# Optimization experiments

Hardware: AMD Instinct MI355X
Metric: run time of the kernel (lower is better)

The kernel has to match this reference:

```python
import jax, jax.numpy as jnp
import numpy as np

B, NV, NL, D, H = 32, 512, 256, 1024, 4096


def _ffn(x, w1, b1, w2, b2):
    # torch FFN: linear2(relu(linear1(x))); weights stored as [in, out]
    return jnp.maximum(x @ w1 + b1, 0.0) @ w2 + b2


def setup_inputs() -> dict:
    key = jax.random.key(0)
    ks = jax.random.split(key, 12)
    s_in = 1.0 / np.sqrt(D)
    s_h = 1.0 / np.sqrt(H)
    return {
        "V": jax.random.normal(ks[0], (B, NV, D), jnp.float32),
        "L": jax.random.normal(ks[1], (B, NL, D), jnp.float32),
        "v_mask": jnp.ones((B, NV), jnp.float32),
        "l_mask": jnp.ones((B, NL), jnp.float32),
        "w1_V": jax.random.normal(ks[2], (D, H), jnp.float32) * s_in,
        "b1_V": jnp.zeros((H,), jnp.float32),
        "w2_V": jax.random.normal(ks[3], (H, D), jnp.float32) * s_h,
        "b2_V": jnp.zeros((D,), jnp.float32),
        "w1_L": jax.random.normal(ks[4], (D, H), jnp.float32) * s_in,
        "b1_L": jnp.zeros((H,), jnp.float32),
        "w2_L": jax.random.normal(ks[5], (H, D), jnp.float32) * s_h,
        "b2_L": jnp.zeros((D,), jnp.float32),
    }


def reference(V, L, v_mask, l_mask, w1_V, b1_V, w2_V, b2_V, w1_L, b1_L, w2_L, b2_L):
    # masks are unused in the original forward
    fV_V = _ffn(V, w1_V, b1_V, w2_V, b2_V)  # [B, NV, D] = ffn_V(V)
    fL_L = _ffn(L, w1_L, b1_L, w2_L, b2_L)  # [B, NL, D] = ffn_L(L)
    fL_V = _ffn(V, w1_L, b1_L, w2_L, b2_L)  # [B, NV, D] = ffn_L(V) (as in source)
    scale = 1.0 / jnp.sqrt(jnp.asarray(V.shape[-1], V.dtype))
    A_LV = jnp.einsum('bnd,bmd->bnm', fV_V, fL_L) * scale  # [B, NV, NL]
    A_VV = jnp.einsum('bnd,bmd->bnm', fV_V, fL_V) * scale  # [B, NV, NV]
    A = jnp.concatenate([A_LV, A_VV], axis=-1)             # [B, NV, NL+NV]
    # softmax over dim=1 (rows), as in the source
    attn = jax.nn.softmax(A, axis=1)
    KV = jnp.concatenate([fL_L, fV_V], axis=1)              # [B, NL+NV, D]
    V_next = jnp.einsum('bnk,bkd->bnd', attn, KV)           # [B, NV, D]
    return (A, V_next)
```

## Files before the change

kernel.cpp:

```cpp
#include <hip/hip_runtime.h>
#include <stdint.h>

#define B_   32
#define NV_  512
#define NL_  256
#define D_   1024
#define H_   4096
#define KTOT 768
#define SCALE_ 0.03125f

typedef __attribute__((ext_vector_type(8))) __bf16 bf8_t;
typedef __attribute__((ext_vector_type(4))) float f32x4;

__device__ __forceinline__ unsigned short f2bf(float f) {
    unsigned u = __float_as_uint(f);
    u += 0x7FFFu + ((u >> 16) & 1u);
    return (unsigned short)(u >> 16);
}
__device__ __forceinline__ unsigned pk2(float lo, float hi) {
    return (unsigned)f2bf(lo) | ((unsigned)f2bf(hi) << 16);
}

__device__ __forceinline__ void gl_lds16(const void* g, const void* lds) {
    __builtin_amdgcn_global_load_lds(
        (const __attribute__((address_space(1))) unsigned int*)(uintptr_t)g,
        (__attribute__((address_space(3))) unsigned int*)(unsigned)(uintptr_t)lds,
        16, 0, 0);
}

#define SBAR() asm volatile("s_barrier" ::: "memory")
#define VMC4() asm volatile("s_waitcnt vmcnt(4)" ::: "memory")
#define VMC0() asm volatile("s_waitcnt vmcnt(0)" ::: "memory")

template<int EPI>
__global__ __launch_bounds__(512, 1)
void gemm256(const unsigned short* __restrict__ Ab, long sAz, int lda,
             const unsigned short* __restrict__ Bb, long sBz, int ldb,
             const float* __restrict__ bias,
             unsigned short* __restrict__ Cp, long sCz, int ldc, int K,
             int nx, int ntile, int tpc)
{
    extern __shared__ unsigned char lds[];
    unsigned char* const ldsA = lds;
    unsigned char* const ldsB = lds + 65536;

    const int tid = threadIdx.x;
    const int w = tid >> 6, l = tid & 63;
    const int wr = w >> 2, wc = w & 3;
    const int lrow = l & 15;
    const int kg = l >> 4;

    int t_, z;
    {
        const int bid = blockIdx.x;
        if (tpc > 0) { const int r = bid >> 3, c = bid & 7; z = r / tpc; t_ = c * tpc + r % tpc; }
        else         { z = bid / ntile; t_ = bid - z * ntile; }
    }
    const int n0 = (t_ % nx) * 256, m0 = (t_ / nx) * 256;

    const unsigned short* A  = Ab + (long)z * sAz;
    const unsigned short* Bg = Bb + (long)z * sBz;

    const int srow = tid >> 3;
    const int scol = ((tid & 7) * 8) ^ ((srow & 7) << 3);
    const int ntk = K >> 6;

    const int cs0 = (((l >> 4) * 16)) ^ ((l & 7) << 4);
    const int cs1 = (64 + ((l >> 4) * 16)) ^ ((l & 7) << 4);

    const unsigned short* const sp0 = Bg + (long)(n0 +   0 + srow) * ldb + scol;
    const unsigned short* const sp1 = Bg + (long)(n0 + 128 + srow) * ldb + scol;
    const unsigned short* const sp2 = A  + (long)(m0 +   0 + srow) * lda + scol;
    const unsigned short* const sp3 = A  + (long)(m0 + 128 + srow) * lda + scol;
    const long stB = (long)64 * ldb, stA = (long)64 * lda;

    f32x4 acc[8][4];
#pragma unroll
    for (int i = 0; i < 8; ++i)
#pragma unroll
        for (int j = 0; j < 4; ++j) acc[i][j] = (f32x4){0.f, 0.f, 0.f, 0.f};

#define STG(tau, part) do {                                                   \
        const int buf_ = (tau) & 1;                                           \
        const int kt_ = ((tau) < ntk ? (tau) : ntk - 1);                      \
        if ((part) < 2) {                                                     \
            const unsigned short* s_ = ((part) == 0 ? sp0 : sp1) + (long)kt_ * 64; \
            unsigned char* d_ = ldsB + (buf_ * 2 + (part)) * 16384 + w * 1024;\
            gl_lds16(s_, d_); gl_lds16(s_ + stB, d_ + 8192);                  \
        } else {                                                              \
            const unsigned short* s_ = ((part) == 2 ? sp2 : sp3) + (long)kt_ * 64; \
            unsigned char* d_ = ldsA + (buf_ * 2 + (part) - 2) * 16384 + w * 1024; \
            gl_lds16(s_, d_); gl_lds16(s_ + stA, d_ + 8192);                  \
        } } while (0)

    auto rdA = [&](int buf, int mf, int cs) -> bf8_t {
        return *(const bf8_t*)(ldsA + (buf * 2 + wr) * 16384 + (mf * 16 + lrow) * 128 + cs);
    };
    auto rdB = [&](int buf, int nf, int cs) -> bf8_t {
        return *(const bf8_t*)(ldsB + (buf * 2 + (wc >> 1)) * 16384 +
                               ((wc & 1) * 64 + nf * 16 + lrow) * 128 + cs);
    };

#define MQ(MO, NO, AREG, BREG)                                                \
    _Pragma("unroll")                                                         \
    for (int mf = 0; mf < 4; ++mf)                                            \
    _Pragma("unroll")                                                         \
        for (int nf = 0; nf < 2; ++nf) {                                      \
            acc[(MO)+mf][(NO)+nf] = __builtin_amdgcn_mfma_f32_16x16x32_bf16(  \
                AREG[mf][0], BREG[nf][0], acc[(MO)+mf][(NO)+nf], 0, 0, 0);    \
            acc[(MO)+mf][(NO)+nf] = __builtin_amdgcn_mfma_f32_16x16x32_bf16(  \
                AREG[mf][1], BREG[nf][1], acc[(MO)+mf][(NO)+nf], 0, 0, 0);    \
        }

    STG(0, 0); STG(0, 1); STG(0, 2); STG(0, 3);
    STG(1, 0); STG(1, 1);
    VMC4();
    SBAR();

    bf8_t a0A[4][2], b0A[2][2];
    bf8_t a0B[4][2], b0B[2][2];
    bf8_t a1r[4][2], b1r[2][2];

#pragma unroll
    for (int mf = 0; mf < 4; ++mf) { a0A[mf][0] = rdA(0, mf, cs0);
                                     a0A[mf][1] = rdA(0, mf, cs1); }
#pragma unroll
    for (int nf = 0; nf < 2; ++nf) { b0A[nf][0] = rdB(0, nf, cs0);
                                     b0A[nf][1] = rdB(0, nf, cs1); }

#define TILEX(BUF, A0C, B0C, A0N, B0N, TAU)                                   \
    STG((TAU) + 1, 2); STG((TAU) + 1, 3);                                     \
    __builtin_amdgcn_s_setprio(1);                                            \
    _Pragma("unroll")                                                         \
    for (int mf = 0; mf < 4; ++mf) { a1r[mf][0] = rdA(BUF, mf + 4, cs0);      \
                                     a1r[mf][1] = rdA(BUF, mf + 4, cs1); }    \
    _Pragma("unroll")                                                         \
    for (int nf = 0; nf < 2; ++nf) { b1r[nf][0] = rdB(BUF, nf + 2, cs0);      \
                                     b1r[nf][1] = rdB(BUF, nf + 2, cs1); }    \
    MQ(0, 0, A0C, B0C)                                                        \
    MQ(0, 2, A0C, b1r)                                                        \
    __builtin_amdgcn_s_setprio(0);                                            \
    SBAR();                                            \
    STG((TAU) + 2, 0); STG((TAU) + 2, 1);                                     \
    VMC4();                                                                   \
    SBAR();                                       \
    __builtin_amdgcn_s_setprio(1);                                            \
    _Pragma("unroll")                                                         \
    for (int mf = 0; mf < 4; ++mf) { A0N[mf][0] = rdA((BUF) ^ 1, mf, cs0);    \
                                     A0N[mf][1] = rdA((BUF) ^ 1, mf, cs1); }  \
    _Pragma("unroll")                                                         \
    for (int nf = 0; nf < 2; ++nf) { B0N[nf][0] = rdB((BUF) ^ 1, nf, cs0);    \
                                     B0N[nf][1] = rdB((BUF) ^ 1, nf, cs1); }  \
    MQ(4, 0, a1r, B0C)                                                        \
    MQ(4, 2, a1r, b1r)                                                        \
    __builtin_amdgcn_s_setprio(0);                                            \
    SBAR();

    for (int t = 0; t < ntk; t += 2) {
        TILEX(0, a0A, b0A, a0B, b0B, t)
        TILEX(1, a0B, b0B, a0A, b0A, t + 1)
    }
#undef TILEX
#undef MQ
#undef STG

    VMC0();
    SBAR();

    unsigned short* C = Cp + (long)z * sCz;
    unsigned char* const scr = lds + w * 16384;

    float bv[4];
#pragma unroll
    for (int nf = 0; nf < 4; ++nf) bv[nf] = bias[n0 + wc * 64 + nf * 16 + lrow];

#pragma unroll
    for (int p = 0; p < 2; ++p) {
#pragma unroll
        for (int mf = 0; mf < 4; ++mf)
#pragma unroll
            for (int nf = 0; nf < 4; ++nf)
#pragma unroll
                for (int r = 0; r < 4; ++r) {
                    float v = acc[4 * p + mf][nf][r] + bv[nf];
                    if (EPI == 0) v = fmaxf(v, 0.f);
                    *(unsigned short*)(scr + (mf * 16 + kg * 4 + r) * 136 +
                                       (nf * 16 + lrow) * 2) = f2bf(v);
                }
#pragma unroll
        for (int it = 0; it < 8; ++it) {
            const int rr = it * 8 + (l >> 3);
            const uint4 q = *(const uint4*)(scr + rr * 136 + (l & 7) * 16);
            *(uint4*)(C + (long)(m0 + wr * 128 + p * 64 + rr) * ldc +
                      (n0 + wc * 64 + (l & 7) * 8)) = q;
        }
    }
}

__device__ __forceinline__ void supertile(int nx, int tpc, int& n0, int& m0, int& z)
{
    const int bid = blockIdx.x;
    const int r = bid >> 3, c = bid & 7;
    z = r / tpc;
    const int t = c * tpc + (r % tpc);
    n0 = (t % nx) * 128;
    m0 = (t / nx) * 128;
}

template<int EPI>
__global__ __launch_bounds__(256)
void mgemm(const unsigned short* __restrict__ Ab, long sAz, int lda,
           const unsigned short* __restrict__ Bb, long sBz, int ldb,
           const float* __restrict__ bias, float scale,
           void* __restrict__ Cp, long sCz, int ldc, int K,
           int nx, int tpc)
{
    __shared__ unsigned short As[128 * 32];
    __shared__ unsigned short Bs[128 * 32];

    const int tid = threadIdx.x;
    const int w = tid >> 6, l = tid & 63;
    const int wr = w >> 1, wc = w & 1;
    const int l15 = l & 15, kg = l >> 4;
    const int srow = l >> 2, scol = (l & 3) * 8;
    int n0, m0, z;
    supertile(nx, tpc, n0, m0, z);

    const unsigned short* A  = Ab + (long)z * sAz;
    const unsigned short* Bg = Bb + (long)z * sBz;

    f32x4 acc[4][4];
#pragma unroll
    for (int m = 0; m < 4; ++m)
#pragma unroll
        for (int n = 0; n < 4; ++n) acc[m][n] = (f32x4){0.f, 0.f, 0.f, 0.f};

    for (int k0 = 0; k0 < K; k0 += 32) {
#pragma unroll
        for (int i = 0; i < 2; ++i) {
            const int g = i * 4 + w;
            gl_lds16(A  + (long)(m0 + g * 16 + srow) * lda + (k0 + scol), &As[g * 512]);
            gl_lds16(Bg + (long)(n0 + g * 16 + srow) * ldb + (k0 + scol), &Bs[g * 512]);
        }
        __syncthreads();

        bf8_t af[4], bf[4];
#pragma unroll
        for (int m = 0; m < 4; ++m)
            af[m] = *(const bf8_t*)&As[(wr * 64 + m * 16 + l15) * 32 + kg * 8];
#pragma unroll
        for (int n = 0; n < 4; ++n)
            bf[n] = *(const bf8_t*)&Bs[(wc * 64 + n * 16 + l15) * 32 + kg * 8];
#pragma unroll
        for (int m = 0; m < 4; ++m)
#pragma unroll
            for (int n = 0; n < 4; ++n)
                acc[m][n] = __builtin_amdgcn_mfma_f32_16x16x32_bf16(af[m], bf[n], acc[m][n], 0, 0, 0);
        __syncthreads();
    }

    const int orow = wr * 64 + (l >> 4) * 4;
    const int ocol = wc * 64 + l15;
    if (EPI == 2) {
        float* C = (float*)Cp + (long)z * sCz;
#pragma unroll
        for (int m = 0; m < 4; ++m)
#pragma unroll
            for (int n = 0; n < 4; ++n)
#pragma unroll
                for (int r = 0; r < 4; ++r)
                    C[(long)(m0 + orow + m * 16 + r) * ldc + (n0 + ocol + n * 16)] =
                        acc[m][n][r] * scale;
    } else {
        unsigned short* C = (unsigned short*)Cp + (long)z * sCz;
#pragma unroll
        for (int n = 0; n < 4; ++n) {
            const float bvv = bias[n0 + ocol + n * 16];
#pragma unroll
            for (int m = 0; m < 4; ++m)
#pragma unroll
                for (int r = 0; r < 4; ++r) {
                    float v = acc[m][n][r] + bvv;
                    if (EPI == 0) v = fmaxf(v, 0.f);
                    C[(long)(m0 + orow + m * 16 + r) * ldc + (n0 + ocol + n * 16)] = f2bf(v);
                }
        }
    }
}

__global__ __launch_bounds__(256)
void col_stats(const float* __restrict__ A, float* __restrict__ Mst, float* __restrict__ RS)
{
    __shared__ float red[4][64];
    const int t = threadIdx.x;
    const int kk = t & 63, ng = t >> 6;
    const int k = blockIdx.x * 64 + kk;
    const int z = blockIdx.y;
    const float* base = A + (long)z * NV_ * KTOT + k;
    float m = -3.0e38f;
    for (int n = ng * 128; n < ng * 128 + 128; ++n) m = fmaxf(m, base[(long)n * KTOT]);
    red[ng][kk] = m;
    __syncthreads();
    m = fmaxf(fmaxf(red[0][kk], red[1][kk]), fmaxf(red[2][kk], red[3][kk]));
    float s = 0.f;
    for (int n = ng * 128; n < ng * 128 + 128; ++n) s += __expf(base[(long)n * KTOT] - m);
    __syncthreads();
    red[ng][kk] = s;
    __syncthreads();
    if (ng == 0) {
        s = red[0][kk] + red[1][kk] + red[2][kk] + red[3][kk];
        Mst[(long)z * KTOT + k] = m;
        RS[(long)z * KTOT + k]  = 1.f / s;
    }
}

__global__ __launch_bounds__(256)
void attn_mfma(const float* __restrict__ Ap, const unsigned short* __restrict__ KVt,
               const float* __restrict__ Mstp, const float* __restrict__ RSp,
               float* __restrict__ Cp, int nx, int tpc)
{
    __shared__ unsigned short As[128 * 32];
    __shared__ unsigned short Bs[128 * 32];

    const int tid = threadIdx.x;
    const int w = tid >> 6, l = tid & 63;
    const int wr = w >> 1, wc = w & 1;
    const int l15 = l & 15, kg = l >> 4;
    const int srow = l >> 2, scol = (l & 3) * 8;
    int n0, m0, z;
    supertile(nx, tpc, n0, m0, z);

    const float* A = Ap + (long)z * NV_ * KTOT;
    const unsigned short* Bg = KVt + (long)z * D_ * KTOT;
    const float* Mz = Mstp + (long)z * KTOT;
    const float* Rz = RSp  + (long)z * KTOT;
    float* C = Cp + (long)z * NV_ * D_;

    const int ar = tid >> 1;
    const int ah = (tid & 1) * 16;

    f32x4 acc[4][4];
#pragma unroll
    for (int m = 0; m < 4; ++m)
#pragma unroll
        for (int n = 0; n < 4; ++n) acc[m][n] = (f32x4){0.f, 0.f, 0.f, 0.f};

    for (int k0 = 0; k0 < KTOT; k0 += 32) {
#pragma unroll
        for (int i = 0; i < 2; ++i) {
            const int g = i * 4 + w;
            gl_lds16(Bg + (long)(n0 + g * 16 + srow) * KTOT + (k0 + scol), &Bs[g * 512]);
        }
        const float* arow = A + (long)(m0 + ar) * KTOT + k0 + ah;
        const float4 x0 = *(const float4*)(arow);
        const float4 x1 = *(const float4*)(arow + 4);
        const float4 x2 = *(const float4*)(arow + 8);
        const float4 x3 = *(const float4*)(arow + 12);
        const float4 ma = *(const float4*)(Mz + k0 + ah);
        const float4 mb = *(const float4*)(Mz + k0 + ah + 4);
        const float4 mc = *(const float4*)(Mz + k0 + ah + 8);
        const float4 md = *(const float4*)(Mz + k0 + ah + 12);
        const float4 ra = *(const float4*)(Rz + k0 + ah);
        const float4 rb = *(const float4*)(Rz + k0 + ah + 4);
        const float4 rc = *(const float4*)(Rz + k0 + ah + 8);
        const float4 rd = *(const float4*)(Rz + k0 + ah + 12);
        const unsigned q0 = pk2(__expf(x0.x - ma.x) * ra.x, __expf(x0.y - ma.y) * ra.y);
        const unsigned q1 = pk2(__expf(x0.z - ma.z) * ra.z, __expf(x0.w - ma.w) * ra.w);
        const unsigned q2 = pk2(__expf(x1.x - mb.x) * rb.x, __expf(x1.y - mb.y) * rb.y);
        const unsigned q3 = pk2(__expf(x1.z - mb.z) * rb.z, __expf(x1.w - mb.w) * rb.w);
        const unsigned q4 = pk2(__expf(x2.x - mc.x) * rc.x, __expf(x2.y - mc.y) * rc.y);
        const unsigned q5 = pk2(__expf(x2.z - mc.z) * rc.z, __expf(x2.w - mc.w) * rc.w);
        const unsigned q6 = pk2(__expf(x3.x - md.x) * rd.x, __expf(x3.y - md.y) * rd.y);
        const unsigned q7 = pk2(__expf(x3.z - md.z) * rd.z, __expf(x3.w - md.w) * rd.w);
        *(uint4*)&As[ar * 32 + ah]     = make_uint4(q0, q1, q2, q3);
        *(uint4*)&As[ar * 32 + ah + 8] = make_uint4(q4, q5, q6, q7);
        __syncthreads();

        bf8_t af[4], bf[4];
#pragma unroll
        for (int m = 0; m < 4; ++m)
            af[m] = *(const bf8_t*)&As[(wr * 64 + m * 16 + l15) * 32 + kg * 8];
#pragma unroll
        for (int n = 0; n < 4; ++n)
            bf[n] = *(const bf8_t*)&Bs[(wc * 64 + n * 16 + l15) * 32 + kg * 8];
#pragma unroll
        for (int m = 0; m < 4; ++m)
#pragma unroll
            for (int n = 0; n < 4; ++n)
                acc[m][n] = __builtin_amdgcn_mfma_f32_16x16x32_bf16(af[m], bf[n], acc[m][n], 0, 0, 0);
        __syncthreads();
    }

    const int orow = wr * 64 + (l >> 4) * 4;
    const int ocol = wc * 64 + l15;
#pragma unroll
    for (int m = 0; m < 4; ++m)
#pragma unroll
        for (int n = 0; n < 4; ++n)
#pragma unroll
            for (int r = 0; r < 4; ++r)
                C[(long)(m0 + orow + m * 16 + r) * D_ + (n0 + ocol + n * 16)] = acc[m][n][r];
}

__global__ __launch_bounds__(256)
void tr2bf_f(const float* __restrict__ src, long sSz, int ldS,
             unsigned short* __restrict__ dst, long sDz, int ldD)
{
    __shared__ unsigned short T[64][65];
    const int t = threadIdx.x;
    const int rr = t >> 2, cc = (t & 3) * 16;
    const int r0 = blockIdx.x * 64, c0 = blockIdx.y * 64, z = blockIdx.z;
    const float* S = src + (long)z * sSz + (long)(r0 + rr) * ldS + c0 + cc;
    const float4 a = *(const float4*)(S);
    const float4 b = *(const float4*)(S + 4);
    const float4 c = *(const float4*)(S + 8);
    const float4 d = *(const float4*)(S + 12);
    unsigned short* Tr = &T[rr][cc];
    Tr[0] = f2bf(a.x); Tr[1] = f2bf(a.y); Tr[2]  = f2bf(a.z); Tr[3]  = f2bf(a.w);
    Tr[4] = f2bf(b.x); Tr[5] = f2bf(b.y); Tr[6]  = f2bf(b.z); Tr[7]  = f2bf(b.w);
    Tr[8] = f2bf(c.x); Tr[9] = f2bf(c.y); Tr[10] = f2bf(c.z); Tr[11] = f2bf(c.w);
    Tr[12] = f2bf(d.x); Tr[13] = f2bf(d.y); Tr[14] = f2bf(d.z); Tr[15] = f2bf(d.w);
    __syncthreads();
    unsigned short v[16];
#pragma unroll
    for (int j = 0; j < 16; ++j) v[j] = T[cc + j][rr];
    unsigned q[8];
#pragma unroll
    for (int j = 0; j < 8; ++j) q[j] = (unsigned)v[2 * j] | ((unsigned)v[2 * j + 1] << 16);
    unsigned short* Dp = dst + (long)z * sDz + (long)(c0 + rr) * ldD + r0 + cc;
    *(uint4*)Dp       = make_uint4(q[0], q[1], q[2], q[3]);
    *(uint4*)(Dp + 8) = make_uint4(q[4], q[5], q[6], q[7]);
}

__global__ __launch_bounds__(256)
void tr2bf_h(const unsigned short* __restrict__ src, long sSz, int ldS,
             unsigned short* __restrict__ dst, long sDz, int ldD)
{
    __shared__ unsigned short T[64][65];
    const int t = threadIdx.x;
    const int rr = t >> 2, cc = (t & 3) * 16;
    const int r0 = blockIdx.x * 64, c0 = blockIdx.y * 64, z = blockIdx.z;
    const unsigned short* S = src + (long)z * sSz + (long)(r0 + rr) * ldS + c0 + cc;
    const uint4 qa = *(const uint4*)(S);
    const uint4 qb = *(const uint4*)(S + 8);
    unsigned short* Tr = &T[rr][cc];
    Tr[0]  = qa.x & 0xFFFF; Tr[1]  = qa.x >> 16; Tr[2]  = qa.y & 0xFFFF; Tr[3]  = qa.y >> 16;
    Tr[4]  = qa.z & 0xFFFF; Tr[5]  = qa.z >> 16; Tr[6]  = qa.w & 0xFFFF; Tr[7]  = qa.w >> 16;
    Tr[8]  = qb.x & 0xFFFF; Tr[9]  = qb.x >> 16; Tr[10] = qb.y & 0xFFFF; Tr[11] = qb.y >> 16;
    Tr[12] = qb.z & 0xFFFF; Tr[13] = qb.z >> 16; Tr[14] = qb.w & 0xFFFF; Tr[15] = qb.w >> 16;
    __syncthreads();
    unsigned short v[16];
#pragma unroll
    for (int j = 0; j < 16; ++j) v[j] = T[cc + j][rr];
    unsigned q[8];
#pragma unroll
    for (int j = 0; j < 8; ++j) q[j] = (unsigned)v[2 * j] | ((unsigned)v[2 * j + 1] << 16);
    unsigned short* Dp = dst + (long)z * sDz + (long)(c0 + rr) * ldD + r0 + cc;
    *(uint4*)Dp       = make_uint4(q[0], q[1], q[2], q[3]);
    *(uint4*)(Dp + 8) = make_uint4(q[4], q[5], q[6], q[7]);
}

__global__ __launch_bounds__(256)
void cvt_bf(const float* __restrict__ src, unsigned short* __restrict__ dst, long n)
{
    const long i = ((long)blockIdx.x * 256 + threadIdx.x) * 8;
    if (i >= n) return;
    const float4 a = *(const float4*)(src + i);
    const float4 b = *(const float4*)(src + i + 4);
    *(uint4*)(dst + i) = make_uint4(pk2(a.x, a.y), pk2(a.z, a.w), pk2(b.x, b.y), pk2(b.z, b.w));
}

extern "C" void kernel_launch(void* const* d_in, const int* in_sizes, int n_in,
                              void* d_out, int out_size, void* d_ws, size_t ws_size,
                              hipStream_t stream)
{
    (void)in_sizes; (void)n_in; (void)out_size;

    const float* V   = (const float*)d_in[0];
    const float* L   = (const float*)d_in[1];
    const float* w1V = (const float*)d_in[4];
    const float* b1V = (const float*)d_in[5];
    const float* w2V = (const float*)d_in[6];
    const float* b2V = (const float*)d_in[7];
    const float* w1L = (const float*)d_in[8];
    const float* b1L = (const float*)d_in[9];
    const float* w2L = (const float*)d_in[10];
    const float* b2L = (const float*)d_in[11];

    float* outA = (float*)d_out;
    float* outV = outA + (size_t)B_ * NV_ * KTOT;

    unsigned short* w1Vt = (unsigned short*)d_ws;
    unsigned short* w2Vt = w1Vt + (size_t)H_ * D_;
    unsigned short* w1Lt = w2Vt + (size_t)D_ * H_;
    unsigned short* w2Lt = w1Lt + (size_t)H_ * D_;
    unsigned short* pool = w2Lt + (size_t)D_ * H_;

    const size_t perb_us = (size_t)NV_ * D_ + (size_t)NL_ * D_ + (size_t)NV_ * H_ +
                           (size_t)NV_ * D_ + (size_t)NL_ * D_ + (size_t)NV_ * D_ +
                           (size_t)D_ * KTOT;
    const size_t perb_bytes = perb_us * 2 + 2 * (size_t)KTOT * sizeof(float);
    const size_t persist_bytes = (size_t)4 * H_ * D_ * 2;
    const size_t avail = (ws_size > persist_bytes + 256) ? ws_size - persist_bytes - 256 : 0;
    int bc = (int)(avail / perb_bytes);
    if (bc > B_) bc = B_;
    if (bc < 1)  bc = 1;

    unsigned short* Vb  = pool;
    unsigned short* Lb  = Vb  + (size_t)bc * NV_ * D_;
    unsigned short* hid = Lb  + (size_t)bc * NL_ * D_;
    unsigned short* fV  = hid + (size_t)bc * NV_ * H_;
    unsigned short* fLL = fV  + (size_t)bc * NV_ * D_;
    unsigned short* fLV = fLL + (size_t)bc * NL_ * D_;
    unsigned short* KVt = fLV + (size_t)bc * NV_ * D_;
    float* Mst = (float*)(KVt + (size_t)bc * D_ * KTOT);
    float* RS  = Mst + (size_t)bc * KTOT;

    const dim3 blk(256);
    const dim3 blk5(512);

    {
        auto* f0 = gemm256<0>;
        auto* f1 = gemm256<1>;
        hipFuncSetAttribute((const void*)f0, hipFuncAttributeMaxDynamicSharedMemorySize, 131072);
        hipFuncSetAttribute((const void*)f1, hipFuncAttributeMaxDynamicSharedMemorySize, 131072);
    }

    tr2bf_f<<<dim3(D_ / 64, H_ / 64, 1), blk, 0, stream>>>(w1V, 0, H_, w1Vt, 0, D_);
    tr2bf_f<<<dim3(H_ / 64, D_ / 64, 1), blk, 0, stream>>>(w2V, 0, D_, w2Vt, 0, H_);
    tr2bf_f<<<dim3(D_ / 64, H_ / 64, 1), blk, 0, stream>>>(w1L, 0, H_, w1Lt, 0, D_);
    tr2bf_f<<<dim3(H_ / 64, D_ / 64, 1), blk, 0, stream>>>(w2L, 0, D_, w2Lt, 0, H_);

    for (int b0 = 0; b0 < B_; b0 += bc) {
        const int cur = (B_ - b0 < bc) ? (B_ - b0) : bc;

        cvt_bf<<<dim3(cur * NV_ * D_ / 2048), blk, 0, stream>>>(
            V + (size_t)b0 * NV_ * D_, Vb, (long)cur * NV_ * D_);
        cvt_bf<<<dim3(cur * NL_ * D_ / 2048), blk, 0, stream>>>(
            L + (size_t)b0 * NL_ * D_, Lb, (long)cur * NL_ * D_);

        #define G256(M, N) dim3((unsigned)(((N) / 256) * ((M) / 256) * cur)), blk5, 131072, stream
        #define P256(M, N) (N) / 256, (((N) / 256) * ((M) / 256)), \
                           ((((N) / 256) * ((M) / 256)) % 8 == 0 ? (((N) / 256) * ((M) / 256)) / 8 : 0)

        gemm256<0><<<G256(NV_, H_)>>>(Vb, (long)NV_ * D_, D_, w1Vt, 0, D_, b1V,
                                      hid, (long)NV_ * H_, H_, D_, P256(NV_, H_));
        gemm256<1><<<G256(NV_, D_)>>>(hid, (long)NV_ * H_, H_, w2Vt, 0, H_, b2V,
                                      fV, (long)NV_ * D_, D_, H_, P256(NV_, D_));
        gemm256<0><<<G256(NL_, H_)>>>(Lb, (long)NL_ * D_, D_, w1Lt, 0, D_, b1L,
                                      hid, (long)NV_ * H_, H_, D_, P256(NL_, H_));
        gemm256<1><<<G256(NL_, D_)>>>(hid, (long)NV_ * H_, H_, w2Lt, 0, H_, b2L,
                                      fLL, (long)NL_ * D_, D_, H_, P256(NL_, D_));
        gemm256<0><<<G256(NV_, H_)>>>(Vb, (long)NV_ * D_, D_, w1Lt, 0, D_, b1L,
                                      hid, (long)NV_ * H_, H_, D_, P256(NV_, H_));
        gemm256<1><<<G256(NV_, D_)>>>(hid, (long)NV_ * H_, H_, w2Lt, 0, H_, b2L,
                                      fLV, (long)NV_ * D_, D_, H_, P256(NV_, D_));
        #undef G256
        #undef P256

        #define GRID(nx, ny) dim3((unsigned)((nx) * (ny) * cur)), blk
        #define SWZ(nx, ny)  (nx), ((nx) * (ny) / 8)
        mgemm<2><<<GRID(NL_ / 128, NV_ / 128), 0, stream>>>(
            fV, (long)NV_ * D_, D_, fLL, (long)NL_ * D_, D_, nullptr, SCALE_,
            outA + (size_t)b0 * NV_ * KTOT, (long)NV_ * KTOT, KTOT, D_,
            SWZ(NL_ / 128, NV_ / 128));
        mgemm<2><<<GRID(NV_ / 128, NV_ / 128), 0, stream>>>(
            fV, (long)NV_ * D_, D_, fLV, (long)NV_ * D_, D_, nullptr, SCALE_,
            outA + (size_t)b0 * NV_ * KTOT + NL_, (long)NV_ * KTOT, KTOT, D_,
            SWZ(NV_ / 128, NV_ / 128));

        tr2bf_h<<<dim3(NL_ / 64, D_ / 64, cur), blk, 0, stream>>>(
            fLL, (long)NL_ * D_, D_, KVt, (long)D_ * KTOT, KTOT);
        tr2bf_h<<<dim3(NV_ / 64, D_ / 64, cur), blk, 0, stream>>>(
            fV, (long)NV_ * D_, D_, KVt + NL_, (long)D_ * KTOT, KTOT);

        col_stats<<<dim3(KTOT / 64, cur), blk, 0, stream>>>(
            outA + (size_t)b0 * NV_ * KTOT, Mst, RS);

        attn_mfma<<<GRID(D_ / 128, NV_ / 128), 0, stream>>>(
            outA + (size_t)b0 * NV_ * KTOT, KVt, Mst, RS,
            outV + (size_t)b0 * NV_ * D_, SWZ(D_ / 128, NV_ / 128));
        #undef GRID
        #undef SWZ
    }
}
```

Baseline: 929.7 us.

## Concatenate FFN outputs and compute scores with single large-tile GEMM

FFN second-layer outputs are written straight into concatenated buffers (fL_L then fL_V in one, fL_L then fV_V in the other), with fL_L dual-stored into both. The two score mgemm launches and the two transposes then collapse into one 256-tile gemm256 launch with an fp32 scaled epilogue and one transpose. The gemm256 pipeline now prefetches all four stage chunks of the next tile at once, waiting on vmcnt(8) plus an lgkmcnt(0) wait before the barrier. This removes the smaller, less efficient mgemm kernel and some launches, at the cost of an extra dual store and a different wait pattern in the main loop.

```diff
diff --git a/kernel.cpp b/kernel.cpp
--- a/kernel.cpp
+++ b/kernel.cpp
@@ -29,15 +29,17 @@
 }
 
 #define SBAR() asm volatile("s_barrier" ::: "memory")
-#define VMC4() asm volatile("s_waitcnt vmcnt(4)" ::: "memory")
+#define VMC8() asm volatile("s_waitcnt vmcnt(8)" ::: "memory")
 #define VMC0() asm volatile("s_waitcnt vmcnt(0)" ::: "memory")
+#define LGK0() asm volatile("s_waitcnt lgkmcnt(0)" ::: "memory")
 
 template<int EPI>
 __global__ __launch_bounds__(512, 1)
 void gemm256(const unsigned short* __restrict__ Ab, long sAz, int lda,
              const unsigned short* __restrict__ Bb, long sBz, int ldb,
-             const float* __restrict__ bias,
-             unsigned short* __restrict__ Cp, long sCz, int ldc, int K,
+             const float* __restrict__ bias, float scale,
+             void* __restrict__ Cp, unsigned short* __restrict__ C2p,
+             long sCz, int ldc, int K,
              int nx, int ntile, int tpc)
 {
     extern __shared__ unsigned char lds[];
@@ -113,8 +115,8 @@
         }
 
     STG(0, 0); STG(0, 1); STG(0, 2); STG(0, 3);
-    STG(1, 0); STG(1, 1);
-    VMC4();
+    STG(1, 0); STG(1, 1); STG(1, 2); STG(1, 3);
+    VMC8();
     SBAR();
 
     bf8_t a0A[4][2], b0A[2][2];
@@ -129,7 +131,6 @@
                                      b0A[nf][1] = rdB(0, nf, cs1); }
 
 #define TILEX(BUF, A0C, B0C, A0N, B0N, TAU)                                   \
-    STG((TAU) + 1, 2); STG((TAU) + 1, 3);                                     \
     __builtin_amdgcn_s_setprio(1);                                            \
     _Pragma("unroll")                                                         \
     for (int mf = 0; mf < 4; ++mf) { a1r[mf][0] = rdA(BUF, mf + 4, cs0);      \
@@ -140,10 +141,12 @@
     MQ(0, 0, A0C, B0C)                                                        \
     MQ(0, 2, A0C, b1r)                                                        \
     __builtin_amdgcn_s_setprio(0);                                            \
-    SBAR();                                            \
+    LGK0();                                                                   \
+    SBAR();                                      \
     STG((TAU) + 2, 0); STG((TAU) + 2, 1);                                     \
-    VMC4();                                                                   \
-    SBAR();                                       \
+    STG((TAU) + 2, 2); STG((TAU) + 2, 3);                                     \
+    VMC8();                                          \
+    SBAR();                                                            \
     __builtin_amdgcn_s_setprio(1);                                            \
     _Pragma("unroll")                                                         \
     for (int mf = 0; mf < 4; ++mf) { A0N[mf][0] = rdA((BUF) ^ 1, mf, cs0);    \
@@ -167,7 +170,21 @@
     VMC0();
     SBAR();
 
-    unsigned short* C = Cp + (long)z * sCz;
+    if (EPI == 2) {
+        float* C = (float*)Cp + (long)z * sCz;
+#pragma unroll
+        for (int mf = 0; mf < 8; ++mf)
+#pragma unroll
+            for (int nf = 0; nf < 4; ++nf)
+#pragma unroll
+                for (int r = 0; r < 4; ++r)
+                    C[(long)(m0 + wr * 128 + mf * 16 + kg * 4 + r) * ldc +
+                      (n0 + wc * 64 + nf * 16 + lrow)] = acc[mf][nf][r] * scale;
+        return;
+    }
+
+    unsigned short* C  = (unsigned short*)Cp + (long)z * sCz;
+    unsigned short* C2 = C2p ? (C2p + (long)z * sCz) : nullptr;
     unsigned char* const scr = lds + w * 16384;
 
     float bv[4];
@@ -191,8 +208,10 @@
         for (int it = 0; it < 8; ++it) {
             const int rr = it * 8 + (l >> 3);
             const uint4 q = *(const uint4*)(scr + rr * 136 + (l & 7) * 16);
-            *(uint4*)(C + (long)(m0 + wr * 128 + p * 64 + rr) * ldc +
-                      (n0 + wc * 64 + (l & 7) * 8)) = q;
+            const long off = (long)(m0 + wr * 128 + p * 64 + rr) * ldc +
+                             (n0 + wc * 64 + (l & 7) * 8);
+            *(uint4*)(C + off) = q;
+            if (C2) *(uint4*)(C2 + off) = q;
         }
     }
 }
@@ -205,87 +224,6 @@
     const int t = c * tpc + (r % tpc);
     n0 = (t % nx) * 128;
     m0 = (t / nx) * 128;
-}
-
-template<int EPI>
-__global__ __launch_bounds__(256)
-void mgemm(const unsigned short* __restrict__ Ab, long sAz, int lda,
-           const unsigned short* __restrict__ Bb, long sBz, int ldb,
-           const float* __restrict__ bias, float scale,
-           void* __restrict__ Cp, long sCz, int ldc, int K,
-           int nx, int tpc)
-{
-    __shared__ unsigned short As[128 * 32];
-    __shared__ unsigned short Bs[128 * 32];
-
-    const int tid = threadIdx.x;
-    const int w = tid >> 6, l = tid & 63;
-    const int wr = w >> 1, wc = w & 1;
-    const int l15 = l & 15, kg = l >> 4;
-    const int srow = l >> 2, scol = (l & 3) * 8;
-    int n0, m0, z;
-    supertile(nx, tpc, n0, m0, z);
-
-    const unsigned short* A  = Ab + (long)z * sAz;
-    const unsigned short* Bg = Bb + (long)z * sBz;
-
-    f32x4 acc[4][4];
-#pragma unroll
-    for (int m = 0; m < 4; ++m)
-#pragma unroll
-        for (int n = 0; n < 4; ++n) acc[m][n] = (f32x4){0.f, 0.f, 0.f, 0.f};
-
-    for (int k0 = 0; k0 < K; k0 += 32) {
-#pragma unroll
-        for (int i = 0; i < 2; ++i) {
-            const int g = i * 4 + w;
-            gl_lds16(A  + (long)(m0 + g * 16 + srow) * lda + (k0 + scol), &As[g * 512]);
-            gl_lds16(Bg + (long)(n0 + g * 16 + srow) * ldb + (k0 + scol), &Bs[g * 512]);
-        }
-        __syncthreads();
-
-        bf8_t af[4], bf[4];
-#pragma unroll
-        for (int m = 0; m < 4; ++m)
-            af[m] = *(const bf8_t*)&As[(wr * 64 + m * 16 + l15) * 32 + kg * 8];
-#pragma unroll
-        for (int n = 0; n < 4; ++n)
-            bf[n] = *(const bf8_t*)&Bs[(wc * 64 + n * 16 + l15) * 32 + kg * 8];
-#pragma unroll
-        for (int m = 0; m < 4; ++m)
-#pragma unroll
-            for (int n = 0; n < 4; ++n)
-                acc[m][n] = __builtin_amdgcn_mfma_f32_16x16x32_bf16(af[m], bf[n], acc[m][n], 0, 0, 0);
-        __syncthreads();
-    }
-
-    const int orow = wr * 64 + (l >> 4) * 4;
-    const int ocol = wc * 64 + l15;
-    if (EPI == 2) {
-        float* C = (float*)Cp + (long)z * sCz;
-#pragma unroll
-        for (int m = 0; m < 4; ++m)
-#pragma unroll
-            for (int n = 0; n < 4; ++n)
-#pragma unroll
-                for (int r = 0; r < 4; ++r)
-                    C[(long)(m0 + orow + m * 16 + r) * ldc + (n0 + ocol + n * 16)] =
-                        acc[m][n][r] * scale;
-    } else {
-        unsigned short* C = (unsigned short*)Cp + (long)z * sCz;
-#pragma unroll
-        for (int n = 0; n < 4; ++n) {
-            const float bvv = bias[n0 + ocol + n * 16];
-#pragma unroll
-            for (int m = 0; m < 4; ++m)
-#pragma unroll
-                for (int r = 0; r < 4; ++r) {
-                    float v = acc[m][n][r] + bvv;
-                    if (EPI == 0) v = fmaxf(v, 0.f);
-                    C[(long)(m0 + orow + m * 16 + r) * ldc + (n0 + ocol + n * 16)] = f2bf(v);
-                }
-        }
-    }
 }
 
 __global__ __launch_bounds__(256)
@@ -497,8 +435,7 @@
     unsigned short* pool = w2Lt + (size_t)D_ * H_;
 
     const size_t perb_us = (size_t)NV_ * D_ + (size_t)NL_ * D_ + (size_t)NV_ * H_ +
-                           (size_t)NV_ * D_ + (size_t)NL_ * D_ + (size_t)NV_ * D_ +
-                           (size_t)D_ * KTOT;
+                           3ul * KTOT * D_;
     const size_t perb_bytes = perb_us * 2 + 2 * (size_t)KTOT * sizeof(float);
     const size_t persist_bytes = (size_t)4 * H_ * D_ * 2;
     const size_t avail = (ws_size > persist_bytes + 256) ? ws_size - persist_bytes - 256 : 0;
@@ -506,13 +443,12 @@
     if (bc > B_) bc = B_;
     if (bc < 1)  bc = 1;
 
-    unsigned short* Vb  = pool;
-    unsigned short* Lb  = Vb  + (size_t)bc * NV_ * D_;
-    unsigned short* hid = Lb  + (size_t)bc * NL_ * D_;
-    unsigned short* fV  = hid + (size_t)bc * NV_ * H_;
-    unsigned short* fLL = fV  + (size_t)bc * NV_ * D_;
-    unsigned short* fLV = fLL + (size_t)bc * NL_ * D_;
-    unsigned short* KVt = fLV + (size_t)bc * NV_ * D_;
+    unsigned short* Vb   = pool;
+    unsigned short* Lb   = Vb   + (size_t)bc * NV_ * D_;
+    unsigned short* hid  = Lb   + (size_t)bc * NL_ * D_;
+    unsigned short* fCat = hid  + (size_t)bc * NV_ * H_;
+    unsigned short* KCat = fCat + (size_t)bc * KTOT * D_;
+    unsigned short* KVt  = KCat + (size_t)bc * KTOT * D_;
     float* Mst = (float*)(KVt + (size_t)bc * D_ * KTOT);
     float* RS  = Mst + (size_t)bc * KTOT;
 
@@ -522,8 +458,10 @@
     {
         auto* f0 = gemm256<0>;
         auto* f1 = gemm256<1>;
+        auto* f2 = gemm256<2>;
         hipFuncSetAttribute((const void*)f0, hipFuncAttributeMaxDynamicSharedMemorySize, 131072);
         hipFuncSetAttribute((const void*)f1, hipFuncAttributeMaxDynamicSharedMemorySize, 131072);
+        hipFuncSetAttribute((const void*)f2, hipFuncAttributeMaxDynamicSharedMemorySize, 131072);
     }
 
     tr2bf_f<<<dim3(D_ / 64, H_ / 64, 1), blk, 0, stream>>>(w1V, 0, H_, w1Vt, 0, D_);
@@ -543,44 +481,37 @@
         #define P256(M, N) (N) / 256, (((N) / 256) * ((M) / 256)), \
                            ((((N) / 256) * ((M) / 256)) % 8 == 0 ? (((N) / 256) * ((M) / 256)) / 8 : 0)
 
-        gemm256<0><<<G256(NV_, H_)>>>(Vb, (long)NV_ * D_, D_, w1Vt, 0, D_, b1V,
-                                      hid, (long)NV_ * H_, H_, D_, P256(NV_, H_));
-        gemm256<1><<<G256(NV_, D_)>>>(hid, (long)NV_ * H_, H_, w2Vt, 0, H_, b2V,
-                                      fV, (long)NV_ * D_, D_, H_, P256(NV_, D_));
-        gemm256<0><<<G256(NL_, H_)>>>(Lb, (long)NL_ * D_, D_, w1Lt, 0, D_, b1L,
-                                      hid, (long)NV_ * H_, H_, D_, P256(NL_, H_));
-        gemm256<1><<<G256(NL_, D_)>>>(hid, (long)NV_ * H_, H_, w2Lt, 0, H_, b2L,
-                                      fLL, (long)NL_ * D_, D_, H_, P256(NL_, D_));
-        gemm256<0><<<G256(NV_, H_)>>>(Vb, (long)NV_ * D_, D_, w1Lt, 0, D_, b1L,
-                                      hid, (long)NV_ * H_, H_, D_, P256(NV_, H_));
-        gemm256<1><<<G256(NV_, D_)>>>(hid, (long)NV_ * H_, H_, w2Lt, 0, H_, b2L,
-                                      fLV, (long)NV_ * D_, D_, H_, P256(NV_, D_));
+        gemm256<0><<<G256(NV_, H_)>>>(Vb, (long)NV_ * D_, D_, w1Vt, 0, D_, b1V, 0.f,
+                                      hid, nullptr, (long)NV_ * H_, H_, D_, P256(NV_, H_));
+        gemm256<1><<<G256(NV_, D_)>>>(hid, (long)NV_ * H_, H_, w2Vt, 0, H_, b2V, 0.f,
+                                      KCat + (size_t)NL_ * D_, nullptr,
+                                      (long)KTOT * D_, D_, H_, P256(NV_, D_));
+        gemm256<0><<<G256(NL_, H_)>>>(Lb, (long)NL_ * D_, D_, w1Lt, 0, D_, b1L, 0.f,
+                                      hid, nullptr, (long)NV_ * H_, H_, D_, P256(NL_, H_));
+        gemm256<1><<<G256(NL_, D_)>>>(hid, (long)NV_ * H_, H_, w2Lt, 0, H_, b2L, 0.f,
+                                      fCat, KCat, (long)KTOT * D_, D_, H_, P256(NL_, D_));
+        gemm256<0><<<G256(NV_, H_)>>>(Vb, (long)NV_ * D_, D_, w1Lt, 0, D_, b1L, 0.f,
+                                      hid, nullptr, (long)NV_ * H_, H_, D_, P256(NV_, H_));
+        gemm256<1><<<G256(NV_, D_)>>>(hid, (long)NV_ * H_, H_, w2Lt, 0, H_, b2L, 0.f,
+                                      fCat + (size_t)NL_ * D_, nullptr,
+                                      (long)KTOT * D_, D_, H_, P256(NV_, D_));
+
+        gemm256<2><<<G256(NV_, KTOT)>>>(KCat + (size_t)NL_ * D_, (long)KTOT * D_, D_,
+                                        fCat, (long)KTOT * D_, D_, nullptr, SCALE_,
+                                        outA + (size_t)b0 * NV_ * KTOT, nullptr,
+                                        (long)NV_ * KTOT, KTOT, D_, P256(NV_, KTOT));
         #undef G256
         #undef P256
 
-        #define GRID(nx, ny) dim3((unsigned)((nx) * (ny) * cur)), blk
-        #define SWZ(nx, ny)  (nx), ((nx) * (ny) / 8)
-        mgemm<2><<<GRID(NL_ / 128, NV_ / 128), 0, stream>>>(
-            fV, (long)NV_ * D_, D_, fLL, (long)NL_ * D_, D_, nullptr, SCALE_,
-            outA + (size_t)b0 * NV_ * KTOT, (long)NV_ * KTOT, KTOT, D_,
-            SWZ(NL_ / 128, NV_ / 128));
-        mgemm<2><<<GRID(NV_ / 128, NV_ / 128), 0, stream>>>(
-            fV, (long)NV_ * D_, D_, fLV, (long)NV_ * D_, D_, nullptr, SCALE_,
-            outA + (size_t)b0 * NV_ * KTOT + NL_, (long)NV_ * KTOT, KTOT, D_,
-            SWZ(NV_ / 128, NV_ / 128));
-
-        tr2bf_h<<<dim3(NL_ / 64, D_ / 64, cur), blk, 0, stream>>>(
-            fLL, (long)NL_ * D_, D_, KVt, (long)D_ * KTOT, KTOT);
-        tr2bf_h<<<dim3(NV_ / 64, D_ / 64, cur), blk, 0, stream>>>(
-            fV, (long)NV_ * D_, D_, KVt + NL_, (long)D_ * KTOT, KTOT);
+        tr2bf_h<<<dim3(KTOT / 64, D_ / 64, cur), blk, 0, stream>>>(
+            KCat, (long)KTOT * D_, D_, KVt, (long)D_ * KTOT, KTOT);
 
         col_stats<<<dim3(KTOT / 64, cur), blk, 0, stream>>>(
             outA + (size_t)b0 * NV_ * KTOT, Mst, RS);
 
-        attn_mfma<<<GRID(D_ / 128, NV_ / 128), 0, stream>>>(
+        attn_mfma<<<dim3((unsigned)((D_ / 128) * (NV_ / 128) * cur)), blk, 0, stream>>>(
             outA + (size_t)b0 * NV_ * KTOT, KVt, Mst, RS,
-            outV + (size_t)b0 * NV_ * D_, SWZ(D_ / 128, NV_ / 128));
-        #undef GRID
-        #undef SWZ
-    }
-}
+            outV + (size_t)b0 * NV_ * D_,
+            D_ / 128, (D_ / 128) * (NV_ / 128) / 8);
+    }
+}
```

Result: slower. 961.5 us (+3.4%).
